# Kernel optimization log

Hardware: AMD Instinct MI355X
Metric: run time of the kernel (lower is better)

The kernel has to match this reference:

```python
import jax, jax.numpy as jnp
import numpy as np

DIM, N_HEADS, N_KV, HEAD_DIM = 4096, 32, 8, 128
N_REP = N_HEADS // N_KV
MAX_BS, MAX_SEQ = 2, 2048
ROPE_THETA = 500000.0


def setup_inputs() -> dict:
    key = jax.random.key(0)
    ks = jax.random.split(key, 6)
    b, s = 2, 2048
    x = jax.random.normal(ks[0], (b, s, DIM), dtype=jnp.float32)
    # weights stored like nn.Linear: [out, in]
    sc = 1.0 / np.sqrt(DIM)
    wq = jax.random.normal(ks[1], (N_HEADS * HEAD_DIM, DIM), dtype=jnp.float32) * sc
    wk = jax.random.normal(ks[2], (N_KV * HEAD_DIM, DIM), dtype=jnp.float32) * sc
    wv = jax.random.normal(ks[3], (N_KV * HEAD_DIM, DIM), dtype=jnp.float32) * sc
    wo = jax.random.normal(ks[4], (DIM, N_HEADS * HEAD_DIM), dtype=jnp.float32) * sc
    # rotary tables (real/imag of freq_complex)
    t = jnp.arange(s, dtype=jnp.float32)
    inv = ROPE_THETA ** (-jnp.arange(0, HEAD_DIM, 2, dtype=jnp.float32) / HEAD_DIM)
    ang = t[:, None] * inv[None, :]  # [s, head_dim/2]
    freqs_cos = jnp.cos(ang)
    freqs_sin = jnp.sin(ang)
    cache_k = jnp.zeros((MAX_BS, MAX_SEQ, N_KV, HEAD_DIM), dtype=jnp.float32)
    cache_v = jnp.zeros((MAX_BS, MAX_SEQ, N_KV, HEAD_DIM), dtype=jnp.float32)
    return {"x": x, "wq": wq, "wk": wk, "wv": wv, "wo": wo,
            "freqs_cos": freqs_cos, "freqs_sin": freqs_sin,
            "cache_k": cache_k, "cache_v": cache_v, "start_pos": 0}


def _apply_rope(t, cos, sin):
    # t: [b, s, h, hd]; complex rotation over adjacent pairs
    b, s, h, hd = t.shape
    t2 = t.reshape(b, s, h, hd // 2, 2)
    t0, t1 = t2[..., 0], t2[..., 1]
    c = cos[None, :, None, :]
    sn = sin[None, :, None, :]
    o0 = t0 * c - t1 * sn
    o1 = t0 * sn + t1 * c
    return jnp.stack([o0, o1], axis=-1).reshape(b, s, h, hd)


def reference(x, wq, wk, wv, wo, freqs_cos, freqs_sin, cache_k, cache_v, start_pos):
    b, s, _ = x.shape
    xq = (x @ wq.T).reshape(b, s, N_HEADS, HEAD_DIM)
    xk = (x @ wk.T).reshape(b, s, N_KV, HEAD_DIM)
    xv = (x @ wv.T).reshape(b, s, N_KV, HEAD_DIM)
    xq = _apply_rope(xq, freqs_cos, freqs_sin)
    xk = _apply_rope(xk, freqs_cos, freqs_sin)
    # KV-cache append at start_pos
    cache_k = jax.lax.dynamic_update_slice(cache_k, xk, (0, start_pos, 0, 0))
    cache_v = jax.lax.dynamic_update_slice(cache_v, xv, (0, start_pos, 0, 0))
    kv_len = start_pos + s
    keys = cache_k[:b, :kv_len]   # [b, kv, n_kv, hd]
    vals = cache_v[:b, :kv_len]
    # GQA: group query heads instead of repeating K/V (same math as repeat_kv)
    q = xq.reshape(b, s, N_KV, N_REP, HEAD_DIM)
    scores = jnp.einsum('bsgrd,btgd->bgrst', q, keys) / np.sqrt(HEAD_DIM)
    # causal mask: query i (absolute pos start_pos+i) attends to j <= start_pos+i
    qpos = start_pos + jnp.arange(s)
    kpos = jnp.arange(kv_len)
    mask = kpos[None, :] <= qpos[:, None]  # [s, kv]
    scores = jnp.where(mask[None, None, None], scores, -jnp.inf)
    probs = jax.nn.softmax(scores, axis=-1)
    out = jnp.einsum('bgrst,btgd->bsgrd', probs, vals).reshape(b, s, N_HEADS * HEAD_DIM)
    return out @ wo.T
```

## Files before the change

### kernel.cpp

```cpp
#include <hip/hip_runtime.h>
#include <stdint.h>

typedef unsigned short ushort_t;
typedef short v8s __attribute__((ext_vector_type(8)));
typedef short v4s __attribute__((ext_vector_type(4)));
typedef float v4f __attribute__((ext_vector_type(4)));
typedef unsigned int uint32;

#define DIM   4096
#define NH    32
#define NKV   8
#define HD    128
#define SEQ   2048
#define BATCH 2
#define NTOK  (BATCH * SEQ)
#define QKVN  (NH * HD + 2 * NKV * HD)
#define KOFF  (NH * HD)
#define VOFF  (NH * HD + NKV * HD)

__device__ __forceinline__ ushort_t f2bf(float f) {
    uint32 u = __float_as_uint(f);
    u += 0x7fff + ((u >> 16) & 1);
    return (ushort_t)(u >> 16);
}
__device__ __forceinline__ float bf2f(ushort_t h) {
    return __uint_as_float(((uint32)h) << 16);
}
__device__ __forceinline__ void gl2lds16(const void* g, void* l) {
    __builtin_amdgcn_global_load_lds(
        (const __attribute__((address_space(1))) uint32*)g,
        (__attribute__((address_space(3))) uint32*)l, 16, 0, 0);
}
#if __has_builtin(__builtin_amdgcn_exp2f)
__device__ __forceinline__ float fast_exp2(float x) { return __builtin_amdgcn_exp2f(x); }
#else
__device__ __forceinline__ float fast_exp2(float x) { return exp2f(x); }
#endif

#if !defined(__HIP_DEVICE_COMPILE__)
__host__ __device__ static inline v4f MFMA_B16_K16(v4s a, v4s b, v4f c) {
    (void)a; (void)b; return c;
}
#elif __has_builtin(__builtin_amdgcn_mfma_f32_16x16x16_bf16)
#define MFMA_B16_K16(A, B, C) __builtin_amdgcn_mfma_f32_16x16x16_bf16(A, B, C, 0, 0, 0)
#elif __has_builtin(__builtin_amdgcn_mfma_f32_16x16x16bf16_1k)
#define MFMA_B16_K16(A, B, C) __builtin_amdgcn_mfma_f32_16x16x16bf16_1k(A, B, C, 0, 0, 0)
#else
#error "no 16x16x16 bf16 MFMA builtin on device"
#endif

__global__ void cvt_f32_bf16(const float* __restrict__ src,
                             ushort_t* __restrict__ dst, int n4) {
    int i = blockIdx.x * blockDim.x + threadIdx.x;
    if (i >= n4) return;
    float4 v = ((const float4*)src)[i];
    uint32 lo = ((uint32)f2bf(v.y) << 16) | f2bf(v.x);
    uint32 hi = ((uint32)f2bf(v.w) << 16) | f2bf(v.z);
    ((uint2*)dst)[i] = make_uint2(lo, hi);
}

template <int OUT_BF16>
__global__ __launch_bounds__(512, 2) void gemm_bt8(const ushort_t* __restrict__ A,
                                                   const ushort_t* __restrict__ B,
                                                   float* __restrict__ Cf,
                                                   ushort_t* __restrict__ Cb,
                                                   int M, int N, int K) {
    __shared__ ushort_t sm[2][2][16384];
    const int t = threadIdx.x;
    const int w = t >> 6, lane = t & 63;
    const int g8 = lane >> 4, l16 = lane & 15;
    const int wr = w >> 2, wc = w & 3;

    const int gx = gridDim.x;
    const int nwg = gx * gridDim.y;
    const int wg0 = blockIdx.y * gx + blockIdx.x;
    const int swz = (wg0 & 7) * (nwg >> 3) + (wg0 >> 3);
    const int bm = swz % gx, bn = swz / gx;

    const ushort_t* Ab = A + (size_t)bm * 256 * K;
    const ushort_t* Bb = B + (size_t)bn * 256 * K;

    const int prt = t >> 3;
    const int gg  = (t & 7) ^ (prt & 7);
    const int rA0 = prt,                              rA1 = prt + 128;
    const int rB0 = ((prt >> 5) << 6) + (prt & 31),   rB1 = rB0 + 128;

    const int pgk  = g8 ^ (l16 & 7);
    const int aoff = (wr * 64 + l16) * 64;
    const int boff = (wc * 32 + l16) * 64;

#define STAGE_A(buf, ah, k0)                                                   \
  do {                                                                         \
    gl2lds16(&Ab[(size_t)(rA0 + (ah) * 64) * K + (k0) + gg * 8],               \
             &sm[buf][0][(ah) * 8192 + t * 8]);                                \
    gl2lds16(&Ab[(size_t)(rA1 + (ah) * 64) * K + (k0) + gg * 8],               \
             &sm[buf][0][(ah) * 8192 + 4096 + t * 8]);                         \
  } while (0)
#define STAGE_B(buf, bh, k0)                                                   \
  do {                                                                         \
    gl2lds16(&Bb[(size_t)(rB0 + (bh) * 32) * K + (k0) + gg * 8],               \
             &sm[buf][1][(bh) * 8192 + t * 8]);                                \
    gl2lds16(&Bb[(size_t)(rB1 + (bh) * 32) * K + (k0) + gg * 8],               \
             &sm[buf][1][(bh) * 8192 + 4096 + t * 8]);                         \
  } while (0)
#define LD_A(dst, buf, ihi)                                                    \
  do {                                                                         \
    _Pragma("unroll") for (int i_ = 0; i_ < 4; ++i_) {                         \
      (dst)[i_ * 2 + 0] = *(const v8s*)&sm[buf][0][(ihi) * 8192 + aoff + i_ * 1024 + pgk * 8];       \
      (dst)[i_ * 2 + 1] = *(const v8s*)&sm[buf][0][(ihi) * 8192 + aoff + i_ * 1024 + (pgk ^ 4) * 8]; \
    }                                                                          \
  } while (0)
#define LD_B(dst, buf, jhi)                                                    \
  do {                                                                         \
    _Pragma("unroll") for (int j_ = 0; j_ < 2; ++j_) {                         \
      (dst)[j_ * 2 + 0] = *(const v8s*)&sm[buf][1][(jhi) * 8192 + boff + j_ * 1024 + pgk * 8];       \
      (dst)[j_ * 2 + 1] = *(const v8s*)&sm[buf][1][(jhi) * 8192 + boff + j_ * 1024 + (pgk ^ 4) * 8]; \
    }                                                                          \
  } while (0)
#define MM(IHI, JHI, AF, BF)                                                   \
  do {                                                                         \
    __builtin_amdgcn_s_setprio(1);                                             \
    _Pragma("unroll") for (int k_ = 0; k_ < 2; ++k_)                           \
      _Pragma("unroll") for (int i_ = 0; i_ < 4; ++i_)                         \
        _Pragma("unroll") for (int j_ = 0; j_ < 2; ++j_)                       \
          acc[(IHI) * 4 + i_][(JHI) * 2 + j_] =                                \
              __builtin_amdgcn_mfma_f32_16x16x32_bf16(                         \
                  (AF)[i_ * 2 + k_], (BF)[j_ * 2 + k_],                        \
                  acc[(IHI) * 4 + i_][(JHI) * 2 + j_], 0, 0, 0);               \
    __builtin_amdgcn_s_setprio(0);                                             \
  } while (0)

    v4f acc[8][4];
    v4f z = {0.f, 0.f, 0.f, 0.f};
#pragma unroll
    for (int i = 0; i < 8; i++)
#pragma unroll
        for (int j = 0; j < 4; j++) acc[i][j] = z;
    v8s af[8], bl[4], bh_[4];

    STAGE_A(0, 0, 0); STAGE_A(0, 1, 0); STAGE_B(0, 0, 0); STAGE_B(0, 1, 0);
    STAGE_A(1, 0, 64); STAGE_B(1, 1, 64); STAGE_A(1, 1, 64);
    asm volatile("s_waitcnt vmcnt(6)" ::: "memory");
    __builtin_amdgcn_s_barrier();

    const int nk = K >> 6;
    for (int T = 0; T < nk; ++T) {
        const int cb = T & 1;
        const int kp = (T + 2) << 6;
        LD_A(af, cb, 0);
        LD_B(bl, cb, 0);
        if (T + 1 < nk) STAGE_B(cb ^ 1, 0, (T + 1) << 6);
        __builtin_amdgcn_s_barrier();
        asm volatile("s_waitcnt lgkmcnt(0)" ::: "memory");
        MM(0, 0, af, bl);
        __builtin_amdgcn_s_barrier();
        LD_B(bh_, cb, 1);
        if (T + 2 < nk) STAGE_A(cb, 0, kp);
        __builtin_amdgcn_s_barrier();
        asm volatile("s_waitcnt lgkmcnt(0)" ::: "memory");
        MM(0, 1, af, bh_);
        __builtin_amdgcn_s_barrier();
        LD_A(af, cb, 1);
        if (T + 2 < nk) STAGE_B(cb, 1, kp);
        __builtin_amdgcn_s_barrier();
        asm volatile("s_waitcnt lgkmcnt(0)" ::: "memory");
        MM(1, 1, af, bh_);
        __builtin_amdgcn_s_barrier();
        if (T + 2 < nk) STAGE_A(cb, 1, kp);
        if (T < nk - 2) { asm volatile("s_waitcnt vmcnt(6)" ::: "memory"); }
        else            { asm volatile("s_waitcnt vmcnt(0)" ::: "memory"); }
        __builtin_amdgcn_s_barrier();
        MM(1, 0, af, bl);
        __builtin_amdgcn_s_barrier();
    }

#undef STAGE_A
#undef STAGE_B
#undef LD_A
#undef LD_B
#undef MM

    const int rowb = bm * 256 + wr * 128;
    const int colb = bn * 256 + wc * 64;
#pragma unroll
    for (int i = 0; i < 8; i++)
#pragma unroll
        for (int j = 0; j < 4; j++)
#pragma unroll
            for (int r = 0; r < 4; r++) {
                int row = rowb + i * 16 + g8 * 4 + r;
                int col = colb + j * 16 + l16;
                float v = acc[i][j][r];
                if (OUT_BF16)
                    Cb[(size_t)row * N + col] = f2bf(v);
                else
                    Cf[(size_t)row * N + col] = v;
            }
}

__global__ __launch_bounds__(256) void rope_reorg(const ushort_t* __restrict__ qkv,
                                                  const float* __restrict__ fc,
                                                  const float* __restrict__ fs,
                                                  ushort_t* __restrict__ Qo,
                                                  ushort_t* __restrict__ Ko) {
    const int tok = blockIdx.x;
    const int bb = tok >> 11, s = tok & 2047;
    const ushort_t* base = qkv + (size_t)tok * QKVN;
    const int t = threadIdx.x;
    const float qscale = 0.08838834764831845f * 1.4426950408889634f;
    uint32* Qw = (uint32*)Qo;
    uint32* Kw = (uint32*)Ko;
#pragma unroll
    for (int i = 0; i < 8; ++i) {
        int p = i * 256 + t;
        int hh = p >> 6, pi = p & 63;
        float c = fc[s * 64 + pi], sn = fs[s * 64 + pi];
        uint32 u = *(const uint32*)&base[hh * 128 + 2 * pi];
        float t0 = bf2f((ushort_t)(u & 0xffff));
        float t1 = bf2f((ushort_t)(u >> 16));
        float o0 = (t0 * c - t1 * sn) * qscale;
        float o1 = (t0 * sn + t1 * c) * qscale;
        size_t dst = (((size_t)bb * NH + hh) * SEQ + s) * HD + 2 * pi;
        Qw[dst >> 1] = ((uint32)f2bf(o1) << 16) | f2bf(o0);
    }
#pragma unroll
    for (int i = 0; i < 2; ++i) {
        int p = i * 256 + t;
        int hh = p >> 6, pi = p & 63;
        float c = fc[s * 64 + pi], sn = fs[s * 64 + pi];
        uint32 u = *(const uint32*)&base[KOFF + hh * 128 + 2 * pi];
        float t0 = bf2f((ushort_t)(u & 0xffff));
        float t1 = bf2f((ushort_t)(u >> 16));
        float o0 = t0 * c - t1 * sn;
        float o1 = t0 * sn + t1 * c;
        size_t dst = (((size_t)bb * NKV + hh) * SEQ + s) * HD + 2 * pi;
        Kw[dst >> 1] = ((uint32)f2bf(o1) << 16) | f2bf(o0);
    }
}

__global__ __launch_bounds__(256) void v_transpose(const ushort_t* __restrict__ qkv,
                                                   ushort_t* __restrict__ Vt) {
    __shared__ ushort_t tile[64][136];
    const int st = blockIdx.x, kvh = blockIdx.y, bb = blockIdx.z;
    const int t = threadIdx.x;
    const int s0 = st * 64;
#pragma unroll
    for (int i = 0; i < 4; ++i) {
        int c = i * 256 + t;
        int r = c >> 4, col8 = (c & 15) * 8;
        int tok = (bb << 11) + s0 + r;
        *(v8s*)&tile[r][col8] =
            *(const v8s*)&qkv[(size_t)tok * QKVN + VOFF + kvh * 128 + col8];
    }
    __syncthreads();
#pragma unroll
    for (int i = 0; i < 4; ++i) {
        int c = i * 256 + t;
        int d = c >> 3, s8 = (c & 7) * 8;
        ushort_t tmp[8];
#pragma unroll
        for (int j = 0; j < 8; j++) tmp[j] = tile[s8 + j][d];
        *(v8s*)&Vt[(((size_t)bb * NKV + kvh) * HD + d) * SEQ + s0 + s8] =
            *(v8s*)tmp;
    }
}

__global__ __launch_bounds__(256, 4) void attn_kernel(const ushort_t* __restrict__ Q,
                                                      const ushort_t* __restrict__ Kc,
                                                      const ushort_t* __restrict__ Vt,
                                                      ushort_t* __restrict__ Out) {
    __shared__ ushort_t Ks[64 * 128];
    __shared__ ushort_t Vs[128 * 64];
    const int qtb = gridDim.x - 1 - blockIdx.x;
    const int h = blockIdx.y, bb = blockIdx.z;
    const int kvh = h >> 2;
    const int t = threadIdx.x, w = t >> 6, lane = t & 63;
    const int g8 = lane >> 4, l16 = lane & 15;
    const int R = qtb * 64 + w * 16;
    const int qrow = R + l16;

    const size_t qb = (((size_t)bb * NH + h) * SEQ + R) * HD;
    v8s qf[4];
#pragma unroll
    for (int ks = 0; ks < 4; ++ks)
        qf[ks] = *(const v8s*)&Q[qb + (size_t)l16 * HD + ks * 32 + g8 * 8];

    float m_i = -3.0e38f, l_i = 0.f;
    v4f z = {0.f, 0.f, 0.f, 0.f};
    v4f o[8];
#pragma unroll
    for (int n = 0; n < 8; n++) o[n] = z;

    const ushort_t* Kbase = Kc + ((size_t)bb * NKV + kvh) * SEQ * HD;
    const ushort_t* Vbase = Vt + ((size_t)bb * NKV + kvh) * HD * SEQ;

    const int nkt = qtb + 1;
    for (int kt = 0; kt < nkt; ++kt) {
        const int k0 = kt * 64;
        __syncthreads();
        const ushort_t* Kt = Kbase + (size_t)k0 * HD;
#pragma unroll
        for (int i = 0; i < 4; ++i) {
            int c = i * 256 + t;
            int r = c >> 4, cc = (c & 15) ^ (r & 15);
            gl2lds16(&Kt[r * 128 + cc * 8], &Ks[c * 8]);
        }
#pragma unroll
        for (int i = 0; i < 4; ++i) {
            int c = i * 256 + t;
            int d = c >> 3, cc = (c & 7) ^ (d & 7);
            gl2lds16(&Vbase[(size_t)d * SEQ + k0 + cc * 8], &Vs[c * 8]);
        }
        __syncthreads();

        v4f s[4];
#pragma unroll
        for (int j = 0; j < 4; j++) s[j] = z;
#pragma unroll
        for (int j = 0; j < 4; j++)
#pragma unroll
            for (int ks = 0; ks < 4; ks++) {
                const v8s kb = *(const v8s*)&Ks[((j * 16 + l16) * 16 + ((ks * 4 + g8) ^ l16)) * 8];
                s[j] = __builtin_amdgcn_mfma_f32_16x16x32_bf16(kb, qf[ks], s[j], 0, 0, 0);
            }

        if (kt == nkt - 1) {
#pragma unroll
            for (int j = 0; j < 4; j++)
#pragma unroll
                for (int r = 0; r < 4; r++) {
                    int key = k0 + j * 16 + g8 * 4 + r;
                    if (key > qrow) s[j][r] = -3.0e38f;
                }
        }

        float mx = fmaxf(fmaxf(s[0][0], s[0][1]), fmaxf(s[0][2], s[0][3]));
#pragma unroll
        for (int j = 1; j < 4; j++)
            mx = fmaxf(mx, fmaxf(fmaxf(s[j][0], s[j][1]), fmaxf(s[j][2], s[j][3])));
        mx = fmaxf(mx, __shfl_xor(mx, 16, 64));
        mx = fmaxf(mx, __shfl_xor(mx, 32, 64));
        float mnew = fmaxf(m_i, mx);
        float alpha = fast_exp2(m_i - mnew);
        m_i = mnew;

        float sum = 0.f;
        v4s pj[4];
#pragma unroll
        for (int j = 0; j < 4; j++)
#pragma unroll
            for (int r = 0; r < 4; r++) {
                float p = fast_exp2(s[j][r] - m_i);
                sum += p;
                pj[j][r] = (short)f2bf(p);
            }
        sum += __shfl_xor(sum, 16, 64);
        sum += __shfl_xor(sum, 32, 64);
        l_i = l_i * alpha + sum;

        float alo[4];
#pragma unroll
        for (int r = 0; r < 4; r++) alo[r] = __shfl(alpha, g8 * 4 + r, 64);
#pragma unroll
        for (int n = 0; n < 8; n++)
#pragma unroll
            for (int r = 0; r < 4; r++) o[n][r] *= alo[r];

#pragma unroll
        for (int j = 0; j < 4; j++)
#pragma unroll
            for (int n = 0; n < 8; n++) {
                const int d = n * 16 + l16;
                const v4s vb = *(const v4s*)&Vs[d * 64 + (((j * 2 + (g8 >> 1)) ^ (l16 & 7)) * 8) + (g8 & 1) * 4];
                o[n] = MFMA_B16_K16(pj[j], vb, o[n]);
            }
    }

    float lo[4];
#pragma unroll
    for (int r = 0; r < 4; r++) lo[r] = __shfl(l_i, g8 * 4 + r, 64);
#pragma unroll
    for (int n = 0; n < 8; n++)
#pragma unroll
        for (int r = 0; r < 4; r++) {
            int row = R + g8 * 4 + r;
            int col = n * 16 + l16;
            Out[(((size_t)bb * SEQ + row) * NH + h) * HD + col] = f2bf(o[n][r] / lo[r]);
        }
}

extern "C" void kernel_launch(void* const* d_in, const int* in_sizes, int n_in,
                              void* d_out, int out_size, void* d_ws, size_t ws_size,
                              hipStream_t stream) {
    const float* x  = (const float*)d_in[0];
    const float* wq = (const float*)d_in[1];
    const float* wk = (const float*)d_in[2];
    const float* wv = (const float*)d_in[3];
    const float* wo = (const float*)d_in[4];
    const float* fc = (const float*)d_in[5];
    const float* fs = (const float*)d_in[6];
    float* out = (float*)d_out;

    ushort_t* ws = (ushort_t*)d_ws;
    size_t off = 0;
    ushort_t* xb    = ws + off; off += (size_t)NTOK * DIM;
    ushort_t* wqkvb = ws + off; off += (size_t)QKVN * DIM;
    ushort_t* wob   = ws + off; off += (size_t)DIM * DIM;
    ushort_t* qkv   = ws + off; off += (size_t)NTOK * QKVN;
    ushort_t* Qb    = ws + off; off += (size_t)BATCH * NH * SEQ * HD;
    ushort_t* Kb    = ws + off; off += (size_t)BATCH * NKV * SEQ * HD;
    ushort_t* Vt    = ws + off; off += (size_t)BATCH * NKV * HD * SEQ;
    ushort_t* attn_out = xb;

    cvt_f32_bf16<<<(NTOK * DIM / 4) / 256, 256, 0, stream>>>(x, xb, NTOK * DIM / 4);
    cvt_f32_bf16<<<(DIM * DIM / 4) / 256, 256, 0, stream>>>(wq, wqkvb, DIM * DIM / 4);
    cvt_f32_bf16<<<(NKV * HD * DIM / 4) / 256, 256, 0, stream>>>(
        wk, wqkvb + (size_t)KOFF * DIM, NKV * HD * DIM / 4);
    cvt_f32_bf16<<<(NKV * HD * DIM / 4) / 256, 256, 0, stream>>>(
        wv, wqkvb + (size_t)VOFF * DIM, NKV * HD * DIM / 4);
    cvt_f32_bf16<<<(DIM * DIM / 4) / 256, 256, 0, stream>>>(wo, wob, DIM * DIM / 4);

    dim3 g1(NTOK / 256, QKVN / 256);
    gemm_bt8<1><<<g1, 512, 0, stream>>>(xb, wqkvb, nullptr, qkv, NTOK, QKVN, DIM);

    rope_reorg<<<NTOK, 256, 0, stream>>>(qkv, fc, fs, Qb, Kb);
    dim3 gv(SEQ / 64, NKV, BATCH);
    v_transpose<<<gv, 256, 0, stream>>>(qkv, Vt);

    dim3 ga(SEQ / 64, NH, BATCH);
    attn_kernel<<<ga, 256, 0, stream>>>(Qb, Kb, Vt, attn_out);

    dim3 g2(NTOK / 256, DIM / 256);
    gemm_bt8<0><<<g2, 512, 0, stream>>>(attn_out, wob, out, nullptr, NTOK, DIM, DIM);
}
```

Measured before the change: 853.6 us.

## Unroll GEMM K-loop by two with ping-pong B fragments and fewer barriers

```diff
diff --git a/kernel.cpp b/kernel.cpp
--- a/kernel.cpp
+++ b/kernel.cpp
@@ -130,48 +130,53 @@
     __builtin_amdgcn_s_setprio(0);                                             \
   } while (0)
 
+#define TILE_BODY(T, BF, BL, BH)                                               \
+  do {                                                                         \
+    const int Tp1 = (T) + 1, Tp2 = (T) + 2;                                    \
+              \
+    LD_A(af, BF, 0);                                                           \
+    LD_B(BH, BF, 1);                                                           \
+    if (Tp1 < nk) STAGE_B((BF) ^ 1, 1, Tp1 << 6);                              \
+    MM(0, 0, af, BL);                                                          \
+    __builtin_amdgcn_s_barrier();                                              \
+                                             \
+    if (Tp2 < nk) STAGE_A(BF, 0, Tp2 << 6);                                    \
+    MM(0, 1, af, BH);                                                          \
+    __builtin_amdgcn_s_barrier();                                              \
+                                             \
+    LD_A(af, BF, 1);                                                           \
+    if (Tp2 < nk) STAGE_B(BF, 0, Tp2 << 6);                                    \
+    MM(1, 1, af, BH);                                                          \
+    __builtin_amdgcn_s_barrier();                                              \
+          \
+    if (Tp2 < nk) STAGE_A(BF, 1, Tp2 << 6);                                    \
+    if ((T) < nk - 2) { asm volatile("s_waitcnt vmcnt(6)" ::: "memory"); }     \
+    else              { asm volatile("s_waitcnt vmcnt(0)" ::: "memory"); }     \
+    __builtin_amdgcn_s_barrier();                                              \
+    if (Tp1 < nk) LD_B(BH, (BF) ^ 1, 0);     \
+    MM(1, 0, af, BL);                                                          \
+            \
+  } while (0)
+
     v4f acc[8][4];
     v4f z = {0.f, 0.f, 0.f, 0.f};
 #pragma unroll
     for (int i = 0; i < 8; i++)
 #pragma unroll
         for (int j = 0; j < 4; j++) acc[i][j] = z;
-    v8s af[8], bl[4], bh_[4];
-
-    STAGE_A(0, 0, 0); STAGE_A(0, 1, 0); STAGE_B(0, 0, 0); STAGE_B(0, 1, 0);
-    STAGE_A(1, 0, 64); STAGE_B(1, 1, 64); STAGE_A(1, 1, 64);
+    v8s af[8], b0[4], b1[4];
+
+    const int nk = K >> 6;
+
+    STAGE_A(0, 0, 0);  STAGE_B(0, 0, 0);  STAGE_A(0, 1, 0);  STAGE_B(0, 1, 0);
+    STAGE_A(1, 0, 64); STAGE_B(1, 0, 64); STAGE_A(1, 1, 64);
     asm volatile("s_waitcnt vmcnt(6)" ::: "memory");
     __builtin_amdgcn_s_barrier();
-
-    const int nk = K >> 6;
-    for (int T = 0; T < nk; ++T) {
-        const int cb = T & 1;
-        const int kp = (T + 2) << 6;
-        LD_A(af, cb, 0);
-        LD_B(bl, cb, 0);
-        if (T + 1 < nk) STAGE_B(cb ^ 1, 0, (T + 1) << 6);
-        __builtin_amdgcn_s_barrier();
-        asm volatile("s_waitcnt lgkmcnt(0)" ::: "memory");
-        MM(0, 0, af, bl);
-        __builtin_amdgcn_s_barrier();
-        LD_B(bh_, cb, 1);
-        if (T + 2 < nk) STAGE_A(cb, 0, kp);
-        __builtin_amdgcn_s_barrier();
-        asm volatile("s_waitcnt lgkmcnt(0)" ::: "memory");
-        MM(0, 1, af, bh_);
-        __builtin_amdgcn_s_barrier();
-        LD_A(af, cb, 1);
-        if (T + 2 < nk) STAGE_B(cb, 1, kp);
-        __builtin_amdgcn_s_barrier();
-        asm volatile("s_waitcnt lgkmcnt(0)" ::: "memory");
-        MM(1, 1, af, bh_);
-        __builtin_amdgcn_s_barrier();
-        if (T + 2 < nk) STAGE_A(cb, 1, kp);
-        if (T < nk - 2) { asm volatile("s_waitcnt vmcnt(6)" ::: "memory"); }
-        else            { asm volatile("s_waitcnt vmcnt(0)" ::: "memory"); }
-        __builtin_amdgcn_s_barrier();
-        MM(1, 0, af, bl);
-        __builtin_amdgcn_s_barrier();
+    LD_B(b0, 0, 0);
+
+    for (int T = 0; T < nk; T += 2) {
+        TILE_BODY(T, 0, b0, b1);
+        TILE_BODY(T + 1, 1, b1, b0);
     }
 
 #undef STAGE_A
@@ -179,6 +184,7 @@
 #undef LD_A
 #undef LD_B
 #undef MM
+#undef TILE_BODY
 
     const int rowb = bm * 256 + wr * 128;
     const int colb = bn * 256 + wc * 64;
```

After: 807.4 us. 5.4% less time.
